# Optimization experiments

Measured on AMD Instinct MI355X. Metric: run time of the kernel, lower is better.

## Reference

```python
import jax, jax.numpy as jnp
import numpy as np

LN_EPS = 1e-12


def _conv1d(x, w, b, pad):
    # x: (B, Cin, L), w: (Cout, Cin, K) -> (B, Cout, L)
    y = jax.lax.conv_general_dilated(x, w, window_strides=(1,), padding=[(pad, pad)],
                                     dimension_numbers=('NCH', 'OIH', 'NCH'))
    return y + b[None, :, None]


def setup_inputs() -> dict:
    key = jax.random.key(0)
    ks = jax.random.split(key, 6)
    B, L, C, KH = 4, 4096, 768, 7
    return {
        'hidden_states': jax.random.normal(ks[0], (B, L, C), jnp.float32),
        'attention_mask': jnp.ones((B, L), jnp.float32),
        'special_tokens_mask': jnp.zeros((B, L), jnp.float32),
        'ln_w': jnp.ones((C,), jnp.float32),
        'ln_b': jnp.zeros((C,), jnp.float32),
        'off_w': jax.random.normal(ks[1], (KH, C, KH), jnp.float32) * 0.02,
        'off_b': jnp.zeros((KH,), jnp.float32),
        'mod_w': jax.random.normal(ks[2], (KH, C, KH), jnp.float32) * 0.02,
        'mod_b': jnp.zeros((KH,), jnp.float32),
        'reg_w': jax.random.normal(ks[3], (C, C, KH), jnp.float32) * 0.02,
    }


def reference(hidden_states, attention_mask, special_tokens_mask,
              ln_w, ln_b, off_w, off_b, mod_w, mod_b, reg_w):
    B, L, C = hidden_states.shape
    kh = off_w.shape[0]
    pad = kh // 2
    residual = hidden_states

    # input layernorm (biased variance, like torch.nn.LayerNorm)
    mu = hidden_states.mean(-1, keepdims=True)
    var = hidden_states.var(-1, keepdims=True)
    h = (hidden_states - mu) * jax.lax.rsqrt(var + LN_EPS) * ln_w + ln_b

    ht = jnp.swapaxes(h, 1, 2)  # (B, C, L)
    off = _conv1d(ht, off_w, off_b, pad)                    # (B, kh, L) seq-axis offsets
    mod = 2.0 * jax.nn.sigmoid(_conv1d(ht, mod_w, mod_b, pad))  # (B, kh, L)

    # mask special tokens / padding before sampling
    gate = ((1.0 - special_tokens_mask) * attention_mask)[:, None, :]
    xm = ht * gate  # (B, C, L)

    # deformable 1D sampling positions: p - pad + k + off[b,k,p]
    base = (jnp.arange(L, dtype=jnp.float32) - pad)[None, :] + jnp.arange(kh, dtype=jnp.float32)[:, None]  # (kh, L)
    pos = base[None, :, :] + off  # (B, kh, L)
    f = jnp.floor(pos)
    t = pos - f                   # (B, kh, L) frac
    fi = f.astype(jnp.int32)

    def gather(idx):
        # linear-sample tap with zero padding outside [0, L-1]
        inb = ((idx >= 0) & (idx <= L - 1)).astype(xm.dtype)  # (B, kh, L)
        idxc = jnp.clip(idx, 0, L - 1)
        v = jax.vmap(lambda xb, ib: xb[:, ib])(xm, idxc)      # (B, C, kh, L)
        return v * inb[:, None, :, :]

    sample = gather(fi) * (1.0 - t)[:, None] + gather(fi + 1) * t[:, None]  # (B, C, kh, L)
    sample = sample * mod[:, None]  # modulated

    out = jnp.einsum('ock,bckp->bop', reg_w, sample)  # (B, C, L)
    out = jnp.swapaxes(out, 1, 2) + residual          # (B, L, C)
    return out
```

## Files before the change

kernel.cpp:

```cpp
#include <hip/hip_runtime.h>
#include <math.h>

#define BB 4
#define LL 4096
#define CC 768
#define KHH 7
#define PADK 3
#define ROWS (BB*LL)
#define NKP  (BB*KHH*LL)
#define GK   (KHH*CC)
#define NT   (GK/64)

typedef unsigned short ushort8 __attribute__((ext_vector_type(8)));
typedef short short8 __attribute__((ext_vector_type(8)));
typedef float f32x4 __attribute__((ext_vector_type(4)));

__device__ __forceinline__ float bf2f(unsigned short u) {
    return __uint_as_float(((unsigned)u) << 16);
}
__device__ __forceinline__ unsigned short f2bf(float x) {
    unsigned u = __float_as_uint(x);
    return (unsigned short)((u + 0x7FFFu + ((u >> 16) & 1u)) >> 16);
}

__global__ __launch_bounds__(256) void k_ln(const float* __restrict__ x,
        const float* __restrict__ mask, const float* __restrict__ special,
        const float* __restrict__ lnw, const float* __restrict__ lnb,
        unsigned short* __restrict__ hb, float* __restrict__ gate) {
    int row = blockIdx.x;
    const float* xr = x + (size_t)row * CC;
    float s = 0.f, q = 0.f;
    for (int i = threadIdx.x; i < CC; i += 256) { float v = xr[i]; s += v; q += v * v; }
    for (int o = 32; o; o >>= 1) { s += __shfl_xor(s, o); q += __shfl_xor(q, o); }
    __shared__ float ss[4], sq[4];
    int wid = threadIdx.x >> 6;
    if ((threadIdx.x & 63) == 0) { ss[wid] = s; sq[wid] = q; }
    __syncthreads();
    s = ss[0] + ss[1] + ss[2] + ss[3];
    q = sq[0] + sq[1] + sq[2] + sq[3];
    float mu  = s * (1.f / CC);
    float var = fmaxf(q * (1.f / CC) - mu * mu, 0.f);
    float rstd = rsqrtf(var + 1e-12f);
    unsigned short* hr = hb + (size_t)row * CC;
    for (int i = threadIdx.x; i < CC; i += 256)
        hr[i] = f2bf((xr[i] - mu) * rstd * lnw[i] + lnb[i]);
    if (threadIdx.x == 0) gate[row] = (1.f - special[row]) * mask[row];
}

__global__ __launch_bounds__(256) void k_wb(const float* __restrict__ rw,
                                            unsigned short* __restrict__ wb) {
    __shared__ float s[GK];
    int o = blockIdx.x;
    for (int i = threadIdx.x; i < GK; i += 256) s[i] = rw[(size_t)o * GK + i];
    __syncthreads();
    unsigned short* orow = wb + (size_t)o * GK;
    for (int f = threadIdx.x; f < GK; f += 256) {
        int k = f / CC, c = f - k * CC;
        orow[f] = f2bf(s[c * KHH + k]);
    }
}

__global__ __launch_bounds__(256) void k_wcb(const float* __restrict__ ow, const float* __restrict__ mw,
                                             unsigned short* __restrict__ wcb) {
    int i = blockIdx.x;
    for (int c = threadIdx.x; c < CC; c += 256) {
        float v = 0.f;
        if (i < 49)      v = ow[(size_t)(i / 7) * (CC * KHH) + (size_t)c * KHH + (i % 7)];
        else if (i < 98) { int j = i - 49; v = mw[(size_t)(j / 7) * (CC * KHH) + (size_t)c * KHH + (j % 7)]; }
        wcb[(size_t)i * CC + c] = f2bf(v);
    }
}

__global__ __launch_bounds__(256) void k_dg2(const unsigned short* __restrict__ A,
        const unsigned short* __restrict__ Bm, float* __restrict__ d) {
    __shared__ __align__(16) char As[128 * 128];
    __shared__ __align__(16) char Bs[128 * 128];
    int r0 = blockIdx.x * 128;
    int t = threadIdx.x;
    int lane = t & 63, w = t >> 6;
    int wr = w >> 1, wc = w & 1;
    f32x4 acc[4][4];
#pragma unroll
    for (int m = 0; m < 4; ++m)
#pragma unroll
        for (int n = 0; n < 4; ++n) acc[m][n] = (f32x4){0.f, 0.f, 0.f, 0.f};
    int lr = lane & 15;
    int lkb0 = (lane >> 4) * 16;
    for (int kk = 0; kk < CC; kk += 64) {
#pragma unroll
        for (int s = 0; s < 4; ++s) {
            int byteoff = (s * 256 + t) * 16;
            int row = byteoff >> 7;
            int colb = byteoff & 127;
            int sw = (row * 128 + colb) ^ ((row & 7) << 4);
            *(ushort8*)(As + sw) = *(const ushort8*)(A + (size_t)(r0 + row) * CC + kk + (colb >> 1));
            *(ushort8*)(Bs + sw) = *(const ushort8*)(Bm + (size_t)row * CC + kk + (colb >> 1));
        }
        __syncthreads();
#pragma unroll
        for (int ks = 0; ks < 2; ++ks) {
            short8 av[4], bv[4];
            int lkb = lkb0 + ks * 64;
#pragma unroll
            for (int m = 0; m < 4; ++m) {
                int ar = wr * 64 + m * 16 + lr;
                av[m] = *(const short8*)(As + ((ar * 128 + lkb) ^ ((ar & 7) << 4)));
            }
#pragma unroll
            for (int n = 0; n < 4; ++n) {
                int br = wc * 64 + n * 16 + lr;
                bv[n] = *(const short8*)(Bs + ((br * 128 + lkb) ^ ((br & 7) << 4)));
            }
#pragma unroll
            for (int m = 0; m < 4; ++m)
#pragma unroll
                for (int n = 0; n < 4; ++n)
                    acc[m][n] = __builtin_amdgcn_mfma_f32_16x16x32_bf16(av[m], bv[n], acc[m][n], 0, 0, 0);
        }
        __syncthreads();
    }
    int lr4 = (lane >> 4) * 4, lc = lane & 15;
#pragma unroll
    for (int m = 0; m < 4; ++m) {
        int gr = r0 + wr * 64 + m * 16 + lr4;
#pragma unroll
        for (int n = 0; n < 4; ++n) {
            int gc = wc * 64 + n * 16 + lc;
#pragma unroll
            for (int j = 0; j < 4; ++j)
                d[(size_t)(gr + j) * 128 + gc] = acc[m][n][j];
        }
    }
}

__global__ __launch_bounds__(256) void k_off(const float* __restrict__ d,
        const float* __restrict__ offb, const float* __restrict__ modb,
        const float* __restrict__ gate,
        int* __restrict__ idx0, int* __restrict__ idx1,
        float* __restrict__ w0a, float* __restrict__ w1a) {
    int flat = blockIdx.x * 256 + threadIdx.x;
    if (flat >= NKP) return;
    int p = flat & (LL - 1);
    int k = (flat >> 12) % KHH;
    int b = flat / (KHH * LL);
    float offa = offb[k], moda = modb[k];
#pragma unroll
    for (int j = 0; j < KHH; ++j) {
        int q = p + j - PADK;
        if (q >= 0 && q < LL) {
            const float* dr = d + (size_t)(b * LL + q) * 128;
            offa += dr[k * 7 + j];
            moda += dr[49 + k * 7 + j];
        }
    }
    float modv = 2.f / (1.f + expf(-moda));
    float pos = (float)(p - PADK + k) + offa;
    pos = fminf(fmaxf(pos, -1.0e9f), 1.0e9f);
    float f = floorf(pos);
    float tf = pos - f;
    int i0 = (int)f;
    int i1 = i0 + 1;
    float in0 = (i0 >= 0 && i0 < LL) ? 1.f : 0.f;
    float in1 = (i1 >= 0 && i1 < LL) ? 1.f : 0.f;
    int c0 = min(max(i0, 0), LL - 1);
    int c1 = min(max(i1, 0), LL - 1);
    float g0 = gate[b * LL + c0] * in0;
    float g1 = gate[b * LL + c1] * in1;
    w0a[flat] = modv * (1.f - tf) * g0;
    w1a[flat] = modv * tf * g1;
    idx0[flat] = c0;
    idx1[flat] = c1;
}

__global__ __launch_bounds__(512, 2) void k_fgemm(const unsigned short* __restrict__ hb,
        const unsigned short* __restrict__ Wb,
        const int* __restrict__ idx0, const int* __restrict__ idx1,
        const float* __restrict__ w0a, const float* __restrict__ w1a,
        const float* __restrict__ resid, float* __restrict__ out) {
    __shared__ __align__(16) char As[2][128 * 128];
    __shared__ __align__(16) char Bs[2][384 * 128];

    int bid = blockIdx.x;
    int nhalf = (bid & 7) >> 2;
    int rowtile = (bid >> 3) * 4 + (bid & 3);
    int r0 = rowtile * 128;
    int o0 = nhalf * 384;
    int b = r0 >> 12;
    int p0 = r0 & (LL - 1);
    int pbase = ((b * KHH) << 12) + p0;
    const unsigned short* hbB = hb + (size_t)b * LL * CC;
    const unsigned short* wbase = Wb + (size_t)o0 * GK;

    int t = threadIdx.x;
    int lane = t & 63, w = t >> 6;
    int wr = w >> 2, wc = w & 3;

    int arow = t >> 2, aseg = t & 3;
    int acolb = aseg * 32;
    int aswz0 = arow * 128 + (acolb ^ ((arow & 7) << 4));
    int aswz1 = arow * 128 + ((acolb + 16) ^ ((arow & 7) << 4));

    f32x4 acc[4][6];
#pragma unroll
    for (int m = 0; m < 4; ++m)
#pragma unroll
        for (int n = 0; n < 6; ++n) acc[m][n] = (f32x4){0.f, 0.f, 0.f, 0.f};

    int g0 = 0, g1 = 0;
    float wa = 0.f, wbv = 0.f;
    int cur_tap = -1;

    ushort8 la0, la1, la2, la3;
    ushort8 lb0, lb1, lb2, lb3, lb4, lb5;

    auto load_phase = [&](int tap, int c0) {
        if (tap != cur_tap) {
            int pf = pbase + (tap << 12) + arow;
            g0 = idx0[pf]; g1 = idx1[pf];
            wa = w0a[pf];  wbv = w1a[pf];
            cur_tap = tap;
        }
        const unsigned short* s0 = hbB + (size_t)g0 * CC + c0 + aseg * 16;
        const unsigned short* s1 = hbB + (size_t)g1 * CC + c0 + aseg * 16;
        la0 = *(const ushort8*)(s0);
        la1 = *(const ushort8*)(s0 + 8);
        la2 = *(const ushort8*)(s1);
        la3 = *(const ushort8*)(s1 + 8);
        int kk = tap * CC + c0;
        {
            int off0 = (0 * 512 + t) * 16;
            lb0 = *(const ushort8*)(wbase + (size_t)(off0 >> 7) * GK + kk + ((off0 & 127) >> 1));
            int off1 = (1 * 512 + t) * 16;
            lb1 = *(const ushort8*)(wbase + (size_t)(off1 >> 7) * GK + kk + ((off1 & 127) >> 1));
            int off2 = (2 * 512 + t) * 16;
            lb2 = *(const ushort8*)(wbase + (size_t)(off2 >> 7) * GK + kk + ((off2 & 127) >> 1));
            int off3 = (3 * 512 + t) * 16;
            lb3 = *(const ushort8*)(wbase + (size_t)(off3 >> 7) * GK + kk + ((off3 & 127) >> 1));
            int off4 = (4 * 512 + t) * 16;
            lb4 = *(const ushort8*)(wbase + (size_t)(off4 >> 7) * GK + kk + ((off4 & 127) >> 1));
            int off5 = (5 * 512 + t) * 16;
            lb5 = *(const ushort8*)(wbase + (size_t)(off5 >> 7) * GK + kk + ((off5 & 127) >> 1));
        }
    };

    auto write_phase = [&](char* Asb, char* Bsb) {
        ushort8 ra, rb;
#pragma unroll
        for (int e = 0; e < 8; ++e) ra[e] = f2bf(fmaf(wa, bf2f(la0[e]), wbv * bf2f(la2[e])));
#pragma unroll
        for (int e = 0; e < 8; ++e) rb[e] = f2bf(fmaf(wa, bf2f(la1[e]), wbv * bf2f(la3[e])));
        *(ushort8*)(Asb + aswz0) = ra;
        *(ushort8*)(Asb + aswz1) = rb;
#define BWR(i, lbv) { int off = (i * 512 + t) * 16; int brow = off >> 7; int colb = off & 127; \
        *(ushort8*)(Bsb + (brow * 128 + (colb ^ ((brow & 7) << 4)))) = lbv; }
        BWR(0, lb0) BWR(1, lb1) BWR(2, lb2) BWR(3, lb3) BWR(4, lb4) BWR(5, lb5)
#undef BWR
    };

    auto compute = [&](const char* Asb, const char* Bsb) {
        int lr = lane & 15;
        int lkb0 = (lane >> 4) * 16;
        __builtin_amdgcn_s_setprio(1);
#pragma unroll
        for (int ks = 0; ks < 2; ++ks) {
            short8 av[4], bv[6];
            int lkb = lkb0 + ks * 64;
#pragma unroll
            for (int m = 0; m < 4; ++m) {
                int ar = wr * 64 + m * 16 + lr;
                av[m] = *(const short8*)(Asb + ar * 128 + (lkb ^ ((ar & 7) << 4)));
            }
#pragma unroll
            for (int n = 0; n < 6; ++n) {
                int br = wc * 96 + n * 16 + lr;
                bv[n] = *(const short8*)(Bsb + br * 128 + (lkb ^ ((br & 7) << 4)));
            }
#pragma unroll
            for (int m = 0; m < 4; ++m)
#pragma unroll
                for (int n = 0; n < 6; ++n)
                    acc[m][n] = __builtin_amdgcn_mfma_f32_16x16x32_bf16(av[m], bv[n], acc[m][n], 0, 0, 0);
        }
        __builtin_amdgcn_s_setprio(0);
    };

    load_phase(0, 0);
    write_phase(As[0], Bs[0]);
    __syncthreads();

    int tap_n = 0, c0_n = 0;
    for (int s = 0; s < NT; ++s) {
        int cur = s & 1;
        c0_n += 64;
        if (c0_n == CC) { c0_n = 0; ++tap_n; }
        bool more = (s + 1 < NT);
        if (more) load_phase(tap_n, c0_n);
        __builtin_amdgcn_sched_barrier(0);
        compute(As[cur], Bs[cur]);
        __builtin_amdgcn_sched_barrier(0);
        if (more) write_phase(As[cur ^ 1], Bs[cur ^ 1]);
        __syncthreads();
    }

    int lr4 = (lane >> 4) * 4, lc = lane & 15;
#pragma unroll
    for (int m = 0; m < 4; ++m) {
        int gr = r0 + wr * 64 + m * 16 + lr4;
#pragma unroll
        for (int n = 0; n < 6; ++n) {
            int gc = o0 + wc * 96 + n * 16 + lc;
#pragma unroll
            for (int j = 0; j < 4; ++j) {
                size_t idx = (size_t)(gr + j) * CC + gc;
                out[idx] = acc[m][n][j] + resid[idx];
            }
        }
    }
}

extern "C" void kernel_launch(void* const* d_in, const int* in_sizes, int n_in,
                              void* d_out, int out_size, void* d_ws, size_t ws_size,
                              hipStream_t stream) {
    const float* x   = (const float*)d_in[0];
    const float* am  = (const float*)d_in[1];
    const float* stm = (const float*)d_in[2];
    const float* lnw = (const float*)d_in[3];
    const float* lnb = (const float*)d_in[4];
    const float* ow  = (const float*)d_in[5];
    const float* ob  = (const float*)d_in[6];
    const float* mw  = (const float*)d_in[7];
    const float* mb  = (const float*)d_in[8];
    const float* rw  = (const float*)d_in[9];
    float* out = (float*)d_out;

    char* ws = (char*)d_ws;
    size_t off = 0;
    auto carve = [&](size_t bytes) -> char* {
        char* p = ws + off;
        off += (bytes + 255) & ~(size_t)255;
        return p;
    };
    unsigned short* hb  = (unsigned short*)carve((size_t)ROWS * CC * 2);
    unsigned short* wb  = (unsigned short*)carve((size_t)CC * GK * 2);
    unsigned short* wcb = (unsigned short*)carve((size_t)128 * CC * 2);
    float* d    = (float*)carve((size_t)ROWS * 128 * 4);
    float* gate = (float*)carve((size_t)ROWS * 4);
    int*   i0   = (int*)carve((size_t)NKP * 4);
    int*   i1   = (int*)carve((size_t)NKP * 4);
    float* w0   = (float*)carve((size_t)NKP * 4);
    float* w1   = (float*)carve((size_t)NKP * 4);

    k_ln<<<ROWS, 256, 0, stream>>>(x, am, stm, lnw, lnb, hb, gate);
    k_wb<<<CC, 256, 0, stream>>>(rw, wb);
    k_wcb<<<128, 256, 0, stream>>>(ow, mw, wcb);
    k_dg2<<<ROWS / 128, 256, 0, stream>>>(hb, wcb, d);
    k_off<<<NKP / 256, 256, 0, stream>>>(d, ob, mb, gate, i0, i1, w0, w1);
    k_fgemm<<<256, 512, 0, stream>>>(hb, wb, i0, i1, w0, w1, x, out);
}
```

Measured before the change: 216.6 us.

## Load weight fragments directly from global into registers, drop B shared-memory staging

The weight (B) operand tiles are no longer staged through LDS. Each lane loads its MFMA B fragments straight from global memory into registers, double-buffered across the two k-substeps and prefetched for the next tile. This cuts the LDS footprint by 96 KB per block and removes the LDS writes and reads for B. In exchange, weight reuse across the two wave rows now depends on L1/L2 hits, and the global loads sit closer to the MFMAs, so memory latency is less well hidden.

```diff
diff --git a/kernel.cpp b/kernel.cpp
--- a/kernel.cpp
+++ b/kernel.cpp
@@ -178,7 +178,6 @@
         const float* __restrict__ w0a, const float* __restrict__ w1a,
         const float* __restrict__ resid, float* __restrict__ out) {
     __shared__ __align__(16) char As[2][128 * 128];
-    __shared__ __align__(16) char Bs[2][384 * 128];
 
     int bid = blockIdx.x;
     int nhalf = (bid & 7) >> 2;
@@ -194,6 +193,13 @@
     int t = threadIdx.x;
     int lane = t & 63, w = t >> 6;
     int wr = w >> 2, wc = w & 3;
+    int lr = lane & 15;
+    int ke0 = (lane >> 4) * 8;
+
+    const unsigned short* bp[6];
+#pragma unroll
+    for (int n = 0; n < 6; ++n)
+        bp[n] = wbase + (size_t)(wc * 96 + n * 16 + lr) * GK + ke0;
 
     int arow = t >> 2, aseg = t & 3;
     int acolb = aseg * 32;
@@ -211,9 +217,9 @@
     int cur_tap = -1;
 
     ushort8 la0, la1, la2, la3;
-    ushort8 lb0, lb1, lb2, lb3, lb4, lb5;
-
-    auto load_phase = [&](int tap, int c0) {
+    short8 bv0[6], bv1[6];
+
+    auto loadA = [&](int tap, int c0) {
         if (tap != cur_tap) {
             int pf = pbase + (tap << 12) + arow;
             g0 = idx0[pf]; g1 = idx1[pf];
@@ -226,24 +232,9 @@
         la1 = *(const ushort8*)(s0 + 8);
         la2 = *(const ushort8*)(s1);
         la3 = *(const ushort8*)(s1 + 8);
-        int kk = tap * CC + c0;
-        {
-            int off0 = (0 * 512 + t) * 16;
-            lb0 = *(const ushort8*)(wbase + (size_t)(off0 >> 7) * GK + kk + ((off0 & 127) >> 1));
-            int off1 = (1 * 512 + t) * 16;
-            lb1 = *(const ushort8*)(wbase + (size_t)(off1 >> 7) * GK + kk + ((off1 & 127) >> 1));
-            int off2 = (2 * 512 + t) * 16;
-            lb2 = *(const ushort8*)(wbase + (size_t)(off2 >> 7) * GK + kk + ((off2 & 127) >> 1));
-            int off3 = (3 * 512 + t) * 16;
-            lb3 = *(const ushort8*)(wbase + (size_t)(off3 >> 7) * GK + kk + ((off3 & 127) >> 1));
-            int off4 = (4 * 512 + t) * 16;
-            lb4 = *(const ushort8*)(wbase + (size_t)(off4 >> 7) * GK + kk + ((off4 & 127) >> 1));
-            int off5 = (5 * 512 + t) * 16;
-            lb5 = *(const ushort8*)(wbase + (size_t)(off5 >> 7) * GK + kk + ((off5 & 127) >> 1));
-        }
-    };
-
-    auto write_phase = [&](char* Asb, char* Bsb) {
+    };
+
+    auto writeA = [&](char* Asb) {
         ushort8 ra, rb;
 #pragma unroll
         for (int e = 0; e < 8; ++e) ra[e] = f2bf(fmaf(wa, bf2f(la0[e]), wbv * bf2f(la2[e])));
@@ -251,55 +242,59 @@
         for (int e = 0; e < 8; ++e) rb[e] = f2bf(fmaf(wa, bf2f(la1[e]), wbv * bf2f(la3[e])));
         *(ushort8*)(Asb + aswz0) = ra;
         *(ushort8*)(Asb + aswz1) = rb;
-#define BWR(i, lbv) { int off = (i * 512 + t) * 16; int brow = off >> 7; int colb = off & 127; \
-        *(ushort8*)(Bsb + (brow * 128 + (colb ^ ((brow & 7) << 4)))) = lbv; }
-        BWR(0, lb0) BWR(1, lb1) BWR(2, lb2) BWR(3, lb3) BWR(4, lb4) BWR(5, lb5)
-#undef BWR
-    };
-
-    auto compute = [&](const char* Asb, const char* Bsb) {
-        int lr = lane & 15;
-        int lkb0 = (lane >> 4) * 16;
+    };
+
+    auto loadB = [&](int kk, int ks, short8* bv) {
+#pragma unroll
+        for (int n = 0; n < 6; ++n)
+            bv[n] = *(const short8*)(bp[n] + kk + ks * 32);
+    };
+
+    auto computeKS = [&](const char* Asb, int ks, const short8* bv) {
         __builtin_amdgcn_s_setprio(1);
-#pragma unroll
-        for (int ks = 0; ks < 2; ++ks) {
-            short8 av[4], bv[6];
-            int lkb = lkb0 + ks * 64;
-#pragma unroll
-            for (int m = 0; m < 4; ++m) {
-                int ar = wr * 64 + m * 16 + lr;
-                av[m] = *(const short8*)(Asb + ar * 128 + (lkb ^ ((ar & 7) << 4)));
-            }
-#pragma unroll
-            for (int n = 0; n < 6; ++n) {
-                int br = wc * 96 + n * 16 + lr;
-                bv[n] = *(const short8*)(Bsb + br * 128 + (lkb ^ ((br & 7) << 4)));
-            }
-#pragma unroll
-            for (int m = 0; m < 4; ++m)
-#pragma unroll
-                for (int n = 0; n < 6; ++n)
-                    acc[m][n] = __builtin_amdgcn_mfma_f32_16x16x32_bf16(av[m], bv[n], acc[m][n], 0, 0, 0);
-        }
+        short8 av[4];
+        int lkb = ke0 * 2 + ks * 64;
+#pragma unroll
+        for (int m = 0; m < 4; ++m) {
+            int ar = wr * 64 + m * 16 + lr;
+            av[m] = *(const short8*)(Asb + ar * 128 + (lkb ^ ((ar & 7) << 4)));
+        }
+#pragma unroll
+        for (int m = 0; m < 4; ++m)
+#pragma unroll
+            for (int n = 0; n < 6; ++n)
+                acc[m][n] = __builtin_amdgcn_mfma_f32_16x16x32_bf16(av[m], bv[n], acc[m][n], 0, 0, 0);
         __builtin_amdgcn_s_setprio(0);
     };
 
-    load_phase(0, 0);
-    write_phase(As[0], Bs[0]);
+    loadA(0, 0);
+    loadB(0, 0, bv0);
+    writeA(As[0]);
     __syncthreads();
 
-    int tap_n = 0, c0_n = 0;
+    int tap_c = 0, c0_c = 0;
     for (int s = 0; s < NT; ++s) {
         int cur = s & 1;
-        c0_n += 64;
+        int kk_cur = tap_c * CC + c0_c;
+        int tap_n = tap_c, c0_n = c0_c + 64;
         if (c0_n == CC) { c0_n = 0; ++tap_n; }
+        int kk_next = tap_n * CC + c0_n;
         bool more = (s + 1 < NT);
-        if (more) load_phase(tap_n, c0_n);
+
+        if (more) loadA(tap_n, c0_n);
+        loadB(kk_cur, 1, bv1);
         __builtin_amdgcn_sched_barrier(0);
-        compute(As[cur], Bs[cur]);
+        computeKS(As[cur], 0, bv0);
         __builtin_amdgcn_sched_barrier(0);
-        if (more) write_phase(As[cur ^ 1], Bs[cur ^ 1]);
+
+        if (more) loadB(kk_next, 0, bv0);
+        __builtin_amdgcn_sched_barrier(0);
+        computeKS(As[cur], 1, bv1);
+        __builtin_amdgcn_sched_barrier(0);
+
+        if (more) writeA(As[cur ^ 1]);
         __syncthreads();
+        tap_c = tap_n; c0_c = c0_n;
     }
 
     int lr4 = (lane >> 4) * 4, lc = lane & 15;
```

Result: slower. 326.1 us (+50.6%).
